# Performance work log

Hardware: AMD Instinct MI355X
Metric: run time of the kernel (lower is better)

The kernel has to match this reference:

```python
import jax, jax.numpy as jnp
import numpy as np

B, S, E, H = 2, 2048, 1024, 16
HD = E // H
DFF = 4 * E
LN_EPS = 1e-5


def _layernorm(x, g, b):
    mu = jnp.mean(x, axis=-1, keepdims=True)
    var = jnp.mean(jnp.square(x - mu), axis=-1, keepdims=True)
    return (x - mu) * jax.lax.rsqrt(var + LN_EPS) * g + b


def setup_inputs() -> dict:
    key = jax.random.key(0)
    ks = jax.random.split(key, 6)
    inp = {
        "x": jax.random.normal(ks[0], (B, S, E), jnp.float32),
        "ln1_g": jnp.ones((E,), jnp.float32),
        "ln1_b": jnp.zeros((E,), jnp.float32),
        "ln2_g": jnp.ones((E,), jnp.float32),
        "ln2_b": jnp.zeros((E,), jnp.float32),
        # OptimizedPoincareBallLinear init: randn * 0.1, zero bias
        "w_qkv": jax.random.normal(ks[1], (3 * E, E), jnp.float32) * 0.1,
        "b_qkv": jnp.zeros((3 * E,), jnp.float32),
        "w_ao": jax.random.normal(ks[2], (E, E), jnp.float32) * 0.1,
        "b_ao": jnp.zeros((E,), jnp.float32),
        "w_fc": jax.random.normal(ks[3], (DFF, E), jnp.float32) * 0.1,
        "b_fc": jnp.zeros((DFF,), jnp.float32),
        "w_po": jax.random.normal(ks[4], (E, DFF), jnp.float32) * 0.1,
        "b_po": jnp.zeros((E,), jnp.float32),
    }
    return inp


def reference(x, ln1_g, ln1_b, ln2_g, ln2_b, w_qkv, b_qkv, w_ao, b_ao,
              w_fc, b_fc, w_po, b_po):
    # --- attention branch ---
    h = _layernorm(x, ln1_g, ln1_b)
    qkv = h @ w_qkv.T + b_qkv                       # [B,S,3E]
    qkv = qkv.reshape(B, S, H, 3 * HD).transpose(0, 2, 1, 3)  # [B,H,S,3hd]
    q, k, v = jnp.split(qkv, 3, axis=-1)            # each [B,H,S,hd]
    scores = jnp.einsum('bhqd,bhkd->bhqk', q, k) / jnp.sqrt(
        jnp.asarray(HD, jnp.float32))
    causal = jnp.tril(jnp.ones((S, S), bool))        # attn_bias[:, :, :S, :S]
    scores = jnp.where(causal, scores, jnp.finfo(scores.dtype).min)
    attn_w = jax.nn.softmax(scores, axis=-1)         # dropout p=0.1 inactive (eval)
    attn = jnp.einsum('bhqk,bhkd->bhqd', attn_w, v)  # [B,H,S,hd]
    attn = attn.transpose(0, 2, 1, 3).reshape(B, S, E)
    attn = attn @ w_ao.T + b_ao
    x = x + attn
    # --- MLP branch ---
    h2 = _layernorm(x, ln2_g, ln2_b)
    h2 = h2 @ w_fc.T + b_fc
    h2 = jax.nn.gelu(h2, approximate=True)           # GPT-2 gelu_new
    h2 = h2 @ w_po.T + b_po
    x = x + h2
    return x
```

## Files before the change

### kernel.cpp

```cpp
#include <hip/hip_runtime.h>
#include <cstddef>
#include <cstdint>

#define Bc 2
#define Sc 2048
#define Ec 1024
#define Hc 16
#define HDc 64
#define DFFc 4096
#define ROWS (Bc * Sc)

typedef _Float16 half8v __attribute__((ext_vector_type(8)));
typedef _Float16 half4v __attribute__((ext_vector_type(4)));
typedef float f32x4 __attribute__((ext_vector_type(4)));
typedef _Float16 h16;

__device__ inline void gld_lds16(const void* g, void* l) {
    __builtin_amdgcn_global_load_lds(
        (const __attribute__((address_space(1))) void*)g,
        (__attribute__((address_space(3))) void*)l, 16, 0, 0);
}

__device__ inline float gelu_new(float x) {
    float x2 = x * x;
    float u = x * fmaf(0.07135481627362f, x2, 1.5957691216057308f);
    return x / (1.0f + __expf(-u));
}

__global__ __launch_bounds__(256) void cvt4_kernel(
    const float* __restrict__ a,
    const float* __restrict__ b,
    const float* __restrict__ c,
    const float* __restrict__ d,
    h16* __restrict__ out)
{
    int bid = blockIdx.x;
    const float* src;
    size_t obase;
    int base;
    if (bid < 3072)      { src = a; obase = 0;       base = bid; }
    else if (bid < 4096) { src = b; obase = 3145728; base = bid - 3072; }
    else if (bid < 8192) { src = c; obase = 4194304; base = bid - 4096; }
    else                 { src = d; obase = 8388608; base = bid - 8192; }
    int i = base * 1024 + threadIdx.x * 4;
    float4 v = *(const float4*)(src + i);
    half4v o;
    o.x = (h16)v.x; o.y = (h16)v.y; o.z = (h16)v.z; o.w = (h16)v.w;
    *(half4v*)(out + obase + i) = o;
}

__device__ inline float block_sum256(float v, float* sb) {
    #pragma unroll
    for (int o = 32; o > 0; o >>= 1) v += __shfl_down(v, o, 64);
    int lane = threadIdx.x & 63, w = threadIdx.x >> 6;
    if (lane == 0) sb[w] = v;
    __syncthreads();
    float r = sb[0] + sb[1] + sb[2] + sb[3];
    __syncthreads();
    return r;
}

__global__ __launch_bounds__(256) void ln_kernel(const float* __restrict__ x,
                                                 const float* __restrict__ g,
                                                 const float* __restrict__ b,
                                                 h16* __restrict__ out) {
    __shared__ float sb[4];
    int row = blockIdx.x;
    int t = threadIdx.x;
    const float* xr = x + (size_t)row * Ec;
    float4 v = ((const float4*)xr)[t];
    float s = v.x + v.y + v.z + v.w;
    float mu = block_sum256(s, sb) * (1.0f / Ec);
    float dx = v.x - mu, dy = v.y - mu, dz = v.z - mu, dw = v.w - mu;
    float ss = dx * dx + dy * dy + dz * dz + dw * dw;
    float var = block_sum256(ss, sb) * (1.0f / Ec);
    float inv = rsqrtf(var + 1e-5f);
    float4 gv = ((const float4*)g)[t];
    float4 bv = ((const float4*)b)[t];
    half4v o;
    o.x = (h16)(dx * inv * gv.x + bv.x);
    o.y = (h16)(dy * inv * gv.y + bv.y);
    o.z = (h16)(dz * inv * gv.z + bv.z);
    o.w = (h16)(dw * inv * gv.w + bv.w);
    ((half4v*)(out + (size_t)row * Ec))[t] = o;
}

template <int EPI, typename OutT>
__global__ __launch_bounds__(512, 2) void gemm_8w(
    const h16* __restrict__ A, const h16* __restrict__ W,
    const float* __restrict__ bias, const float* __restrict__ R,
    OutT* __restrict__ C, int M, int N, int K)
{
    __shared__ h16 S[4][16384];

    const int tid = threadIdx.x;
    const int lane = tid & 63, wv = tid >> 6;
    const int wm = wv >> 2, wn = wv & 3;
    const int c15 = lane & 15, q = lane >> 4;

    const int nbn = N >> 8;
    const int cpx = gridDim.x >> 3;
    const int wg = ((int)blockIdx.x & 7) * cpx + ((int)blockIdx.x >> 3);
    const int r0 = (wg / nbn) << 8, c0 = (wg % nbn) << 8;

    const int gc8 = (tid & 3) ^ ((tid >> 3) & 3);
    const h16* gA = A + (size_t)(r0 + (tid >> 2)) * K + gc8 * 8;
    const h16* gB = W + (size_t)(c0 + (tid >> 2)) * K + gc8 * 8;
    const size_t hK = (size_t)128 * K;

    int aoff[8], boff[4];
    #pragma unroll
    for (int m = 0; m < 8; ++m) {
        int row = wm * 128 + m * 16 + c15;
        aoff[m] = row * 32 + ((q ^ ((row >> 1) & 3)) << 3);
    }
    #pragma unroll
    for (int n = 0; n < 4; ++n) {
        int row = wn * 64 + n * 16 + c15;
        boff[n] = 8192 + row * 32 + ((q ^ ((row >> 1) & 3)) << 3);
    }

    f32x4 acc[8][4];
    #pragma unroll
    for (int m = 0; m < 8; ++m)
        #pragma unroll
        for (int n = 0; n < 4; ++n)
            acc[m][n] = (f32x4){0.f, 0.f, 0.f, 0.f};

    const int NT = K >> 5;

    auto stage = [&](int tt) {
        h16* b = &S[tt & 3][0];
        const h16* a = gA + tt * 32;
        const h16* w = gB + tt * 32;
        gld_lds16(a,      b + tid * 8);
        gld_lds16(a + hK, b + 4096 + tid * 8);
        gld_lds16(w,      b + 8192 + tid * 8);
        gld_lds16(w + hK, b + 12288 + tid * 8);
    };

    stage(0); stage(1); stage(2);
    asm volatile("s_waitcnt vmcnt(8)" ::: "memory");
    __builtin_amdgcn_s_barrier();

    for (int t = 0; t < NT; ++t) {
        if (t + 3 < NT) stage(t + 3);

        const h16* b = &S[t & 3][0];
        half8v af[8], bf[4];
        #pragma unroll
        for (int m = 0; m < 8; ++m) af[m] = *(const half8v*)(b + aoff[m]);
        #pragma unroll
        for (int n = 0; n < 4; ++n) bf[n] = *(const half8v*)(b + boff[n]);

        __builtin_amdgcn_s_setprio(1);
        #pragma unroll
        for (int m = 0; m < 8; ++m)
            #pragma unroll
            for (int n = 0; n < 4; ++n)
                acc[m][n] = __builtin_amdgcn_mfma_f32_16x16x32_f16(af[m], bf[n], acc[m][n], 0, 0, 0);
        __builtin_amdgcn_s_setprio(0);

        if (t < NT - 1) {
            if (t + 3 < NT)       asm volatile("s_waitcnt vmcnt(8)" ::: "memory");
            else if (t + 3 == NT) asm volatile("s_waitcnt vmcnt(4)" ::: "memory");
            else                  asm volatile("s_waitcnt vmcnt(0)" ::: "memory");
            __builtin_amdgcn_s_barrier();
        }
    }

    float bvs[4];
    #pragma unroll
    for (int n = 0; n < 4; ++n) bvs[n] = bias[c0 + wn * 64 + n * 16 + c15];
    #pragma unroll
    for (int m = 0; m < 8; ++m) {
        #pragma unroll
        for (int n = 0; n < 4; ++n) {
            int col = c0 + wn * 64 + n * 16 + c15;
            #pragma unroll
            for (int r = 0; r < 4; ++r) {
                int row = r0 + wm * 128 + m * 16 + q * 4 + r;
                size_t off = (size_t)row * N + col;
                float v = acc[m][n][r] + bvs[n];
                if (EPI == 1) v += R[off];
                if (EPI == 2) v = gelu_new(v);
                if (sizeof(OutT) == 2) ((h16*)C)[off] = (h16)v;
                else ((float*)C)[off] = v;
            }
        }
    }
}

template <int EPI, typename OutT>
__global__ __launch_bounds__(256) void gemm_k64(
    const h16* __restrict__ A, const h16* __restrict__ W,
    const float* __restrict__ bias, const float* __restrict__ R,
    OutT* __restrict__ C, int M, int N, int K)
{
    __shared__ h16 As[2][2][64 * 32];
    __shared__ h16 Ws[2][2][128 * 32];

    const int t = threadIdx.x;
    const int lane = t & 63, wv = t >> 6;
    const int wm = wv >> 1, wn = wv & 1;
    const int c15 = lane & 15, q = lane >> 4;
    const int id = blockIdx.x;
    const int cx = id & 7;
    const int kq = id >> 3;
    const int bx = kq & 7;
    const int by = ((kq >> 3) << 3) | cx;
    const int row0 = by * 64, col0 = bx * 128;
    const int arow = t >> 2, acol = (t & 3) << 3;

    const h16* ap  = A + (size_t)(row0 + arow) * K + acol;
    const h16* wp0 = W + (size_t)(col0 + arow) * K + acol;
    const h16* wp1 = wp0 + (size_t)64 * K;

    f32x4 acc[2][4];
    #pragma unroll
    for (int i = 0; i < 2; ++i)
        #pragma unroll
        for (int j = 0; j < 4; ++j)
            acc[i][j] = (f32x4){0.f, 0.f, 0.f, 0.f};

    auto stageL = [&](h16 (*asB)[64 * 32], h16 (*wsB)[128 * 32], int koff) {
        #pragma unroll
        for (int kk = 0; kk < 2; ++kk) {
            gld_lds16(ap  + koff + kk * 32, &asB[kk][arow * 32 + acol]);
            gld_lds16(wp0 + koff + kk * 32, &wsB[kk][arow * 32 + acol]);
            gld_lds16(wp1 + koff + kk * 32, &wsB[kk][(64 + arow) * 32 + acol]);
        }
    };
    auto computeL = [&](const h16 (*asB)[64 * 32], const h16 (*wsB)[128 * 32]) {
        #pragma unroll
        for (int kk = 0; kk < 2; ++kk) {
            half8v af[2], bfv[4];
            #pragma unroll
            for (int i = 0; i < 2; ++i)
                af[i] = *(const half8v*)&asB[kk][(wm * 32 + i * 16 + c15) * 32 + q * 8];
            #pragma unroll
            for (int j = 0; j < 4; ++j)
                bfv[j] = *(const half8v*)&wsB[kk][(wn * 64 + j * 16 + c15) * 32 + q * 8];
            #pragma unroll
            for (int i = 0; i < 2; ++i)
                #pragma unroll
                for (int j = 0; j < 4; ++j)
                    acc[i][j] = __builtin_amdgcn_mfma_f32_16x16x32_f16(af[i], bfv[j], acc[i][j], 0, 0, 0);
        }
    };

    stageL(As[0], Ws[0], 0);
    __syncthreads();

    int k0 = 0;
    for (; k0 < K - 128; k0 += 128) {
        stageL(As[1], Ws[1], k0 + 64);
        computeL(As[0], Ws[0]);
        __syncthreads();
        stageL(As[0], Ws[0], k0 + 128);
        computeL(As[1], Ws[1]);
        __syncthreads();
    }
    stageL(As[1], Ws[1], k0 + 64);
    computeL(As[0], Ws[0]);
    __syncthreads();
    computeL(As[1], Ws[1]);

    #pragma unroll
    for (int i = 0; i < 2; ++i) {
        #pragma unroll
        for (int j = 0; j < 4; ++j) {
            int col = col0 + wn * 64 + j * 16 + c15;
            float bv = bias[col];
            #pragma unroll
            for (int r = 0; r < 4; ++r) {
                int row = row0 + wm * 32 + i * 16 + q * 4 + r;
                size_t off = (size_t)row * N + col;
                float v = acc[i][j][r] + bv;
                if (EPI == 1) v += R[off];
                if (EPI == 2) v = gelu_new(v);
                if (sizeof(OutT) == 2) ((h16*)C)[off] = (h16)v;
                else ((float*)C)[off] = v;
            }
        }
    }
}

__global__ __launch_bounds__(256, 4) void attn_mfma(const h16* __restrict__ qkv,
                                                    h16* __restrict__ attn) {
    __shared__ h16 Ks[2][2][64 * 32];
    __shared__ h16 Vt[2][64 * 32];
    __shared__ h16 Ps[4][16 * 72];

    const int t = threadIdx.x;
    const int lane = t & 63, wv = t >> 6;
    const int c15 = lane & 15, q = lane >> 4;
    const int bh = blockIdx.x, b = bh >> 4, h = bh & 15;
    const int ja = 31 - blockIdx.y;
    const int qbase = ja * 64 + wv * 16;
    const int SE = 3 * Ec;
    const size_t hbase = (size_t)b * Sc * SE + (size_t)h * (3 * HDc);

    half8v qf[2];
    #pragma unroll
    for (int kk = 0; kk < 2; ++kk) {
        qf[kk] = *(const half8v*)(qkv + hbase + (size_t)(qbase + c15) * SE + kk * 32 + q * 8);
        qf[kk] *= (h16)0.125f;
    }

    f32x4 O[4];
    #pragma unroll
    for (int n = 0; n < 4; ++n) O[n] = (f32x4){0.f, 0.f, 0.f, 0.f};
    float mi = -3e38f, li = 0.f;

    const int krow = t >> 2, kcol = (t & 3) << 3;
    const int vkey = t & 31, vd0 = (t >> 5) << 3;
    half8v vreg[2];

    auto stageK = [&](int kt, int bf) {
        #pragma unroll
        for (int p = 0; p < 2; ++p)
            gld_lds16(qkv + hbase + (size_t)(kt * 64 + krow) * SE + HDc + p * 32 + kcol,
                      &Ks[bf][p][krow * 32 + kcol]);
    };
    auto loadV = [&](int kt) {
        #pragma unroll
        for (int p = 0; p < 2; ++p)
            vreg[p] = *(const half8v*)(qkv + hbase +
                        (size_t)(kt * 64 + p * 32 + vkey) * SE + 2 * HDc + vd0);
    };
    auto scatV = [&]() {
        #pragma unroll
        for (int p = 0; p < 2; ++p)
            #pragma unroll
            for (int u = 0; u < 8; ++u)
                Vt[p][(vd0 + u) * 32 + vkey] = vreg[p][u];
    };

    stageK(0, 0);
    loadV(0);
    scatV();
    __syncthreads();

    for (int kt = 0; kt <= ja; ++kt) {
        const int bf = kt & 1;
        if (kt < ja) { stageK(kt + 1, bf ^ 1); loadV(kt + 1); }

        f32x4 st[4];
        #pragma unroll
        for (int j = 0; j < 4; ++j) {
            half8v kf0 = *(const half8v*)&Ks[bf][0][(j * 16 + c15) * 32 + q * 8];
            half8v kf1 = *(const half8v*)&Ks[bf][1][(j * 16 + c15) * 32 + q * 8];
            f32x4 z = (f32x4){0.f, 0.f, 0.f, 0.f};
            z = __builtin_amdgcn_mfma_f32_16x16x32_f16(kf0, qf[0], z, 0, 0, 0);
            st[j] = __builtin_amdgcn_mfma_f32_16x16x32_f16(kf1, qf[1], z, 0, 0, 0);
        }

        if (kt == ja) {
            const int rowloc = wv * 16 + c15;
            #pragma unroll
            for (int j = 0; j < 4; ++j)
                #pragma unroll
                for (int r = 0; r < 4; ++r)
                    if (j * 16 + q * 4 + r > rowloc) st[j][r] = -3e38f;
        }

        float mx = mi;
        #pragma unroll
        for (int j = 0; j < 4; ++j)
            #pragma unroll
            for (int r = 0; r < 4; ++r) mx = fmaxf(mx, st[j][r]);
        mx = fmaxf(mx, __shfl_xor(mx, 16, 64));
        mx = fmaxf(mx, __shfl_xor(mx, 32, 64));
        float al = __expf(mi - mx);
        mi = mx;
        float ps = 0.f;
        #pragma unroll
        for (int j = 0; j < 4; ++j) {
            half4v pk;
            #pragma unroll
            for (int r = 0; r < 4; ++r) {
                float p = __expf(st[j][r] - mx);
                ps += p;
                pk[r] = (h16)p;
            }
            *(half4v*)&Ps[wv][c15 * 72 + j * 16 + q * 4] = pk;
        }
        ps += __shfl_xor(ps, 16, 64);
        ps += __shfl_xor(ps, 32, 64);
        li = li * al + ps;

        half8v pb0 = *(const half8v*)&Ps[wv][c15 * 72 + q * 8];
        half8v pb1 = *(const half8v*)&Ps[wv][c15 * 72 + 32 + q * 8];
        #pragma unroll
        for (int n = 0; n < 4; ++n) {
            #pragma unroll
            for (int r = 0; r < 4; ++r) O[n][r] *= al;
            half8v va0 = *(const half8v*)&Vt[0][(n * 16 + c15) * 32 + q * 8];
            half8v va1 = *(const half8v*)&Vt[1][(n * 16 + c15) * 32 + q * 8];
            O[n] = __builtin_amdgcn_mfma_f32_16x16x32_f16(va0, pb0, O[n], 0, 0, 0);
            O[n] = __builtin_amdgcn_mfma_f32_16x16x32_f16(va1, pb1, O[n], 0, 0, 0);
        }

        if (kt < ja) {
            __syncthreads();
            scatV();
            __syncthreads();
        }
    }

    float rl = 1.0f / li;
    #pragma unroll
    for (int n = 0; n < 4; ++n) {
        half4v o4;
        #pragma unroll
        for (int r = 0; r < 4; ++r) o4[r] = (h16)(O[n][r] * rl);
        *(half4v*)(attn + ((size_t)(b * Sc + qbase + c15)) * Ec + h * HDc + n * 16 + q * 4) = o4;
    }
}

extern "C" void kernel_launch(void* const* d_in, const int* in_sizes, int n_in,
                              void* d_out, int out_size, void* d_ws, size_t ws_size,
                              hipStream_t stream) {
    const float* x     = (const float*)d_in[0];
    const float* ln1_g = (const float*)d_in[1];
    const float* ln1_b = (const float*)d_in[2];
    const float* ln2_g = (const float*)d_in[3];
    const float* ln2_b = (const float*)d_in[4];
    const float* w_qkv = (const float*)d_in[5];
    const float* b_qkv = (const float*)d_in[6];
    const float* w_ao  = (const float*)d_in[7];
    const float* b_ao  = (const float*)d_in[8];
    const float* w_fc  = (const float*)d_in[9];
    const float* b_fc  = (const float*)d_in[10];
    const float* w_po  = (const float*)d_in[11];
    const float* b_po  = (const float*)d_in[12];
    float* out = (float*)d_out;

    char* w = (char*)d_ws;
    h16* wqkv = (h16*)(w);
    h16* wao  = (h16*)(w + 6291456);
    h16* wfc  = (h16*)(w + 8388608);
    h16* wpo  = (h16*)(w + 16777216);
    h16* hb   = (h16*)(w + 25165824);
    h16* qkv  = (h16*)(w + 33554432);
    h16* attn = (h16*)(w + 58720256);
    float* x1 = (float*)(w + 67108864);
    h16* ff   = qkv;

    dim3 blk(256);
    dim3 blk8(512);

    cvt4_kernel<<<dim3(12288), blk, 0, stream>>>(w_qkv, w_ao, w_fc, w_po, wqkv);

    ln_kernel<<<dim3(ROWS), blk, 0, stream>>>(x, ln1_g, ln1_b, hb);
    gemm_8w<0, h16><<<dim3((ROWS / 256) * (3 * Ec / 256)), blk8, 0, stream>>>(
        hb, wqkv, b_qkv, nullptr, qkv, ROWS, 3 * Ec, Ec);
    attn_mfma<<<dim3(Bc * Hc, 32), blk, 0, stream>>>(qkv, attn);
    gemm_k64<1, float><<<dim3(512), blk, 0, stream>>>(
        attn, wao, b_ao, x, x1, ROWS, Ec, Ec);
    ln_kernel<<<dim3(ROWS), blk, 0, stream>>>(x1, ln2_g, ln2_b, hb);
    gemm_8w<2, h16><<<dim3((ROWS / 256) * (DFFc / 256)), blk8, 0, stream>>>(
        hb, wfc, b_fc, nullptr, ff, ROWS, DFFc, Ec);
    gemm_k64<1, float><<<dim3(512), blk, 0, stream>>>(
        ff, wpo, b_po, x1, out, ROWS, Ec, DFFc);
}
```

Measured before the change: 332.6 us.

## Rework gemm_k64 into 4-stage LDS ring with XOR swizzle and fine-grained waits

New measurement: 348.3 us. 1.05x slower.

```diff
diff --git a/kernel.cpp b/kernel.cpp
--- a/kernel.cpp
+++ b/kernel.cpp
@@ -192,13 +192,12 @@
 }
 
 template <int EPI, typename OutT>
-__global__ __launch_bounds__(256) void gemm_k64(
+__global__ __launch_bounds__(256, 2) void gemm_k64(
     const h16* __restrict__ A, const h16* __restrict__ W,
     const float* __restrict__ bias, const float* __restrict__ R,
     OutT* __restrict__ C, int M, int N, int K)
 {
-    __shared__ h16 As[2][2][64 * 32];
-    __shared__ h16 Ws[2][2][128 * 32];
+    __shared__ h16 S[4][6144];
 
     const int t = threadIdx.x;
     const int lane = t & 63, wv = t >> 6;
@@ -210,11 +209,23 @@
     const int bx = kq & 7;
     const int by = ((kq >> 3) << 3) | cx;
     const int row0 = by * 64, col0 = bx * 128;
-    const int arow = t >> 2, acol = (t & 3) << 3;
-
-    const h16* ap  = A + (size_t)(row0 + arow) * K + acol;
-    const h16* wp0 = W + (size_t)(col0 + arow) * K + acol;
-    const h16* wp1 = wp0 + (size_t)64 * K;
+
+    const int gc8 = (t & 3) ^ ((t >> 3) & 3);
+    const h16* gA  = A + (size_t)(row0 + (t >> 2)) * K + gc8 * 8;
+    const h16* gB0 = W + (size_t)(col0 + (t >> 2)) * K + gc8 * 8;
+    const h16* gB1 = gB0 + (size_t)64 * K;
+
+    int aoff[2], boff[4];
+    #pragma unroll
+    for (int i = 0; i < 2; ++i) {
+        int row = wm * 32 + i * 16 + c15;
+        aoff[i] = row * 32 + ((q ^ ((row >> 1) & 3)) << 3);
+    }
+    #pragma unroll
+    for (int j = 0; j < 4; ++j) {
+        int row = wn * 64 + j * 16 + c15;
+        boff[j] = 2048 + row * 32 + ((q ^ ((row >> 1) & 3)) << 3);
+    }
 
     f32x4 acc[2][4];
     #pragma unroll
@@ -223,48 +234,44 @@
         for (int j = 0; j < 4; ++j)
             acc[i][j] = (f32x4){0.f, 0.f, 0.f, 0.f};
 
-    auto stageL = [&](h16 (*asB)[64 * 32], h16 (*wsB)[128 * 32], int koff) {
-        #pragma unroll
-        for (int kk = 0; kk < 2; ++kk) {
-            gld_lds16(ap  + koff + kk * 32, &asB[kk][arow * 32 + acol]);
-            gld_lds16(wp0 + koff + kk * 32, &wsB[kk][arow * 32 + acol]);
-            gld_lds16(wp1 + koff + kk * 32, &wsB[kk][(64 + arow) * 32 + acol]);
-        }
+    const int NT = K >> 5;
+
+    auto stage = [&](int tt) {
+        h16* b = &S[tt & 3][0];
+        gld_lds16(gA  + tt * 32, b + t * 8);
+        gld_lds16(gB0 + tt * 32, b + 2048 + t * 8);
+        gld_lds16(gB1 + tt * 32, b + 4096 + t * 8);
     };
-    auto computeL = [&](const h16 (*asB)[64 * 32], const h16 (*wsB)[128 * 32]) {
-        #pragma unroll
-        for (int kk = 0; kk < 2; ++kk) {
-            half8v af[2], bfv[4];
-            #pragma unroll
-            for (int i = 0; i < 2; ++i)
-                af[i] = *(const half8v*)&asB[kk][(wm * 32 + i * 16 + c15) * 32 + q * 8];
+
+    stage(0); stage(1); stage(2);
+    asm volatile("s_waitcnt vmcnt(6)" ::: "memory");
+    __builtin_amdgcn_s_barrier();
+
+    for (int tt = 0; tt < NT; ++tt) {
+        if (tt + 3 < NT) stage(tt + 3);
+
+        const h16* b = &S[tt & 3][0];
+        half8v af[2], bf[4];
+        #pragma unroll
+        for (int i = 0; i < 2; ++i) af[i] = *(const half8v*)(b + aoff[i]);
+        #pragma unroll
+        for (int j = 0; j < 4; ++j) bf[j] = *(const half8v*)(b + boff[j]);
+
+        __builtin_amdgcn_s_setprio(1);
+        #pragma unroll
+        for (int i = 0; i < 2; ++i)
             #pragma unroll
             for (int j = 0; j < 4; ++j)
-                bfv[j] = *(const half8v*)&wsB[kk][(wn * 64 + j * 16 + c15) * 32 + q * 8];
-            #pragma unroll
-            for (int i = 0; i < 2; ++i)
-                #pragma unroll
-                for (int j = 0; j < 4; ++j)
-                    acc[i][j] = __builtin_amdgcn_mfma_f32_16x16x32_f16(af[i], bfv[j], acc[i][j], 0, 0, 0);
-        }
-    };
-
-    stageL(As[0], Ws[0], 0);
-    __syncthreads();
-
-    int k0 = 0;
-    for (; k0 < K - 128; k0 += 128) {
-        stageL(As[1], Ws[1], k0 + 64);
-        computeL(As[0], Ws[0]);
-        __syncthreads();
-        stageL(As[0], Ws[0], k0 + 128);
-        computeL(As[1], Ws[1]);
-        __syncthreads();
-    }
-    stageL(As[1], Ws[1], k0 + 64);
-    computeL(As[0], Ws[0]);
-    __syncthreads();
-    computeL(As[1], Ws[1]);
+                acc[i][j] = __builtin_amdgcn_mfma_f32_16x16x32_f16(af[i], bf[j], acc[i][j], 0, 0, 0);
+        __builtin_amdgcn_s_setprio(0);
+
+        if (tt < NT - 1) {
+            if (tt + 3 < NT)       asm volatile("s_waitcnt vmcnt(6)" ::: "memory");
+            else if (tt + 3 == NT) asm volatile("s_waitcnt vmcnt(3)" ::: "memory");
+            else                   asm volatile("s_waitcnt vmcnt(0)" ::: "memory");
+            __builtin_amdgcn_s_barrier();
+        }
+    }
 
     #pragma unroll
     for (int i = 0; i < 2; ++i) {
```
